# Kernel tuning notes

Hardware: AMD Instinct MI355X
Metric: run time of the kernel (lower is better)

Reference implementation:

```python
import jax, jax.numpy as jnp
import numpy as np

N_HEAD = 16
ROPE_BASE = 10000.0


def setup_inputs() -> dict:
    key = jax.random.key(0)
    k1, k2, k3 = jax.random.split(key, 3)
    B, T, C = 2, 2048, 2048
    x = jax.random.normal(k1, (B, T, C), dtype=jnp.float32)
    # 0.02 init scale keeps attention logits in a sane range
    w_qkv = jax.random.normal(k2, (3 * C, C), dtype=jnp.float32) * 0.02
    w_proj = jax.random.normal(k3, (C, C), dtype=jnp.float32) * 0.02
    return {"x": x, "w_qkv": w_qkv, "w_proj": w_proj}


def _apply_rope(t, cos, sin):
    # t: [B, T, H, hd]; cos/sin: [T, hd//2]
    B, T, H, hd = t.shape
    ts = t.reshape(B, T, H, hd // 2, 2)
    x0, x1 = ts[..., 0], ts[..., 1]
    c = cos[None, :, None, :]
    s = sin[None, :, None, :]
    out = jnp.stack([x0 * c - x1 * s, x1 * c + x0 * s], axis=-1)
    return out.reshape(B, T, H, hd)


def reference(x, w_qkv, w_proj):
    B, T, C = x.shape
    H = N_HEAD
    hd = C // H

    qkv = x @ w_qkv.T                       # [B, T, 3C]
    q, k, v = jnp.split(qkv, 3, axis=2)
    q = q.reshape(B, T, H, hd)
    k = k.reshape(B, T, H, hd)              # present kv: pre-RoPE k, [B,T,H,hd]
    v = v.reshape(B, T, H, hd).transpose(0, 2, 1, 3)  # [B,H,T,hd]

    # RoPE cache (positions = arange(T) since past_key_value is None)
    theta = 1.0 / (ROPE_BASE ** (jnp.arange(0, hd, 2, dtype=jnp.float32) / hd))
    ang = jnp.arange(T, dtype=jnp.float32)[:, None] * theta[None, :]  # [T, hd//2]
    cos, sin = jnp.cos(ang), jnp.sin(ang)

    qr = _apply_rope(q, cos, sin).transpose(0, 2, 1, 3)  # [B,H,T,hd]
    kr = _apply_rope(k, cos, sin).transpose(0, 2, 1, 3)  # [B,H,T,hd]

    scale = 1.0 / jnp.sqrt(jnp.asarray(hd, dtype=qr.dtype))
    scores = jnp.einsum('bhqd,bhkd->bhqk', qr, kr) * scale  # [B,H,T,T]
    attn = jax.nn.softmax(scores, axis=-1)
    o = jnp.einsum('bhqk,bhkd->bhqd', attn, v)              # [B,H,T,hd]
    y = o.transpose(0, 2, 1, 3).reshape(B, T, C) @ w_proj.T
    return (y, k, v)
```

## Files before the change

kernel.cpp:

```cpp
#include <hip/hip_runtime.h>
#include <math.h>


typedef __bf16 bf16_t;
typedef __bf16 bf16x8 __attribute__((ext_vector_type(8)));
typedef __bf16 bf16x4v __attribute__((ext_vector_type(4)));
typedef float  f32x4  __attribute__((ext_vector_type(4)));

#define B_  2
#define T_  2048
#define C_  2048
#define SLICE_ ((size_t)B_ * T_ * C_)

__device__ __forceinline__ void glds16(const void* g, void* l) {
  __builtin_amdgcn_global_load_lds(
      (__attribute__((address_space(1))) void*)(void*)(const_cast<void*>(g)),
      (__attribute__((address_space(3))) void*)(l), 16, 0, 0);
}

__global__ __launch_bounds__(256) void k_cvt(const float4* __restrict__ in,
                                             bf16x4v* __restrict__ out, int n4) {
  int i = blockIdx.x * 256 + threadIdx.x;
  if (i < n4) {
    float4 v = in[i];
    bf16x4v o;
    o[0] = (bf16_t)v.x; o[1] = (bf16_t)v.y; o[2] = (bf16_t)v.z; o[3] = (bf16_t)v.w;
    out[i] = o;
  }
}

__global__ __launch_bounds__(256) void k_tab(float2* __restrict__ tab) {
  int i = blockIdx.x * 256 + threadIdx.x;
  int t = i >> 6, j = i & 63;
  float thf = (float)pow(10000.0, -(double)(2 * j) / 128.0);
  float angf = (float)t * thf;
  double a = (double)angf;
  tab[i] = make_float2((float)cos(a), (float)sin(a));
}

__global__ __launch_bounds__(256, 2) void k_qkv(
    const bf16_t* __restrict__ X, const bf16_t* __restrict__ W,
    const float2* __restrict__ tab,
    bf16_t* __restrict__ qb, bf16_t* __restrict__ kb, bf16_t* __restrict__ vtb,
    float* __restrict__ kout, float* __restrict__ vout) {
  const int K = 2048;
  __shared__ alignas(16) bf16_t smem[17408];
  bf16_t* As = smem;
  bf16_t* Bs = smem + 8192;
  const int tid = threadIdx.x;
  const int lane = tid & 63, wv = tid >> 6;
  const int wm = wv >> 1, wn = wv & 1;
  const int q4 = lane >> 4, l16 = lane & 15;
  const int m0 = blockIdx.x * 128, n0 = blockIdx.y * 128;

  const bf16_t* Ab = X + (size_t)m0 * K;
  const bf16_t* Wb = W + (size_t)n0 * K;

  f32x4 zero4 = {0.f, 0.f, 0.f, 0.f};
  f32x4 acc[4][4];
#pragma unroll
  for (int i = 0; i < 4; ++i)
#pragma unroll
    for (int j = 0; j < 4; ++j) acc[i][j] = zero4;

  for (int k0 = 0; k0 < K; k0 += 64) {
    __syncthreads();
#pragma unroll
    for (int i = 0; i < 4; ++i) {
      int ci = i * 256 + tid;
      glds16(Ab + (size_t)(ci >> 3) * K + k0 + (((ci & 7) ^ ((ci >> 3) & 7)) << 3),
             &As[(i * 256 + wv * 64) * 8]);
    }
#pragma unroll
    for (int i = 0; i < 4; ++i) {
      int ci = i * 256 + tid;
      glds16(Wb + (size_t)(ci >> 3) * K + k0 + (((ci & 7) ^ ((ci >> 3) & 7)) << 3),
             &Bs[(i * 256 + wv * 64) * 8]);
    }
    __syncthreads();
#pragma unroll
    for (int kk = 0; kk < 2; ++kk) {
      bf16x8 afrag[4], bfrag[4];
#pragma unroll
      for (int mf = 0; mf < 4; ++mf)
        afrag[mf] = *(const bf16x8*)&As[(wm * 64 + mf * 16 + l16) * 64 +
                                        ((((kk << 2) | q4) ^ (l16 & 7)) << 3)];
#pragma unroll
      for (int nf = 0; nf < 4; ++nf)
        bfrag[nf] = *(const bf16x8*)&Bs[(wn * 64 + nf * 16 + l16) * 64 +
                                        ((((kk << 2) | q4) ^ (l16 & 7)) << 3)];
#pragma unroll
      for (int mf = 0; mf < 4; ++mf)
#pragma unroll
        for (int nf = 0; nf < 4; ++nf)
          acc[mf][nf] = __builtin_amdgcn_mfma_f32_16x16x32_bf16(
              afrag[mf], bfrag[nf], acc[mf][nf], 0, 0, 0);
    }
  }

  __syncthreads();
  const int sec = n0 >> 11;
  const int t0 = m0 & 2047, bb = m0 >> 11, h = (n0 & 2047) >> 7;

  if (sec < 2) {
#pragma unroll
    for (int mf = 0; mf < 4; ++mf)
#pragma unroll
      for (int nf = 0; nf < 4; ++nf)
#pragma unroll
        for (int r = 0; r < 4; ++r) {
          int ml = wm * 64 + mf * 16 + q4 * 4 + r;
          int d = wn * 64 + nf * 16 + l16;
          float val = acc[mf][nf][r];
          float partner = __shfl_xor(val, 1);
          float2 cs = tab[(t0 + ml) * 64 + (d >> 1)];
          float rv = (d & 1) ? (val * cs.x + partner * cs.y)
                             : (val * cs.x - partner * cs.y);
          if (sec == 0) rv *= 0.08838834764831845f;
          else kout[(size_t)(m0 + ml) * 2048 + h * 128 + d] = val;
          smem[ml * 136 + d] = (bf16_t)rv;
        }
    __syncthreads();
    bf16_t* dst = (sec == 0 ? qb : kb);
    size_t gbase = ((size_t)(bb * 16 + h) * 2048 + t0) * 128;
#pragma unroll
    for (int i = 0; i < 8; ++i) {
      int ci = i * 256 + tid, ml = ci >> 4, cc = (ci & 15) * 8;
      *(bf16x8*)(dst + gbase + (size_t)ml * 128 + cc) =
          *(const bf16x8*)&smem[ml * 136 + cc];
    }
  } else {
#pragma unroll
    for (int mf = 0; mf < 4; ++mf)
#pragma unroll
      for (int nf = 0; nf < 4; ++nf)
#pragma unroll
        for (int r = 0; r < 4; ++r) {
          int ml = wm * 64 + mf * 16 + q4 * 4 + r;
          int d = wn * 64 + nf * 16 + l16;
          float val = acc[mf][nf][r];
          vout[((size_t)(bb * 16 + h) * 2048 + t0 + ml) * 128 + d] = val;
          smem[d * 136 + ml] = (bf16_t)val;
        }
    __syncthreads();
#pragma unroll
    for (int i = 0; i < 8; ++i) {
      int ci = i * 256 + tid, dr = ci >> 4, cc = (ci & 15) * 8;
      *(bf16x8*)(vtb + ((size_t)((bb * 16 + h) * 128 + dr)) * 2048 + t0 + cc) =
          *(const bf16x8*)&smem[dr * 136 + cc];
    }
  }
}

__global__ __launch_bounds__(256, 2) void k_attn(
    const bf16_t* __restrict__ qb, const bf16_t* __restrict__ kb,
    const bf16_t* __restrict__ vtb, bf16_t* __restrict__ ob) {
  __shared__ alignas(16) bf16_t Ps[128 * 80];
  __shared__ alignas(16) bf16_t Ks[64 * 128];
  __shared__ alignas(16) bf16_t Vts[128 * 64];

  const int tid = threadIdx.x;
  const int lane = tid & 63, wv = tid >> 6;
  const int q4 = lane >> 4, l16 = lane & 15;
  const int bh = blockIdx.x >> 4;
  const int q0 = (blockIdx.x & 15) * 128;

  const bf16_t* Qg = qb + (size_t)bh * T_ * 128 + (size_t)q0 * 128;
  const bf16_t* Kg = kb + (size_t)bh * T_ * 128;
  const bf16_t* Vg = vtb + (size_t)bh * 128 * T_;

  bf16x8 qa[2][4];
#pragma unroll
  for (int mf = 0; mf < 2; ++mf)
#pragma unroll
    for (int kf = 0; kf < 4; ++kf)
      qa[mf][kf] = *(const bf16x8*)(Qg + (size_t)(wv * 32 + mf * 16 + l16) * 128 +
                                    kf * 32 + q4 * 8);

  f32x4 zero4 = {0.f, 0.f, 0.f, 0.f};
  float lrow[2][4];
  f32x4 oacc[2][8];
#pragma unroll
  for (int mf = 0; mf < 2; ++mf) {
#pragma unroll
    for (int r = 0; r < 4; ++r) lrow[mf][r] = 0.f;
#pragma unroll
    for (int nf = 0; nf < 8; ++nf) oacc[mf][nf] = zero4;
  }

  for (int key0 = 0; key0 < T_; key0 += 64) {
    __syncthreads();
#pragma unroll
    for (int i = 0; i < 4; ++i) {
      int ci = i * 256 + tid;
      glds16(Kg + (size_t)(key0 + (ci >> 4)) * 128 +
                 (((ci & 15) ^ ((ci >> 4) & 7)) << 3),
             &Ks[(i * 256 + wv * 64) * 8]);
    }
#pragma unroll
    for (int i = 0; i < 4; ++i) {
      int ci = i * 256 + tid;
      glds16(Vg + (size_t)(ci >> 3) * T_ + key0 +
                 (((ci & 7) ^ ((ci >> 3) & 7)) << 3),
             &Vts[(i * 256 + wv * 64) * 8]);
    }
    __syncthreads();

    f32x4 sacc[2][4];
#pragma unroll
    for (int mf = 0; mf < 2; ++mf)
#pragma unroll
      for (int nf = 0; nf < 4; ++nf) sacc[mf][nf] = zero4;
#pragma unroll
    for (int kf = 0; kf < 4; ++kf) {
      bf16x8 bfrag[4];
#pragma unroll
      for (int nf = 0; nf < 4; ++nf)
        bfrag[nf] = *(const bf16x8*)&Ks[(nf * 16 + l16) * 128 +
                                        ((((kf << 2) | q4) ^ (l16 & 7)) << 3)];
#pragma unroll
      for (int mf = 0; mf < 2; ++mf)
#pragma unroll
        for (int nf = 0; nf < 4; ++nf)
          sacc[mf][nf] = __builtin_amdgcn_mfma_f32_16x16x32_bf16(
              qa[mf][kf], bfrag[nf], sacc[mf][nf], 0, 0, 0);
    }

#pragma unroll
    for (int mf = 0; mf < 2; ++mf) {
#pragma unroll
      for (int r = 0; r < 4; ++r) {
        float p0 = __expf(sacc[mf][0][r]);
        float p1 = __expf(sacc[mf][1][r]);
        float p2 = __expf(sacc[mf][2][r]);
        float p3 = __expf(sacc[mf][3][r]);
        int prow = wv * 32 + mf * 16 + q4 * 4 + r;
        Ps[prow * 80 + 0 + l16]  = (bf16_t)p0;
        Ps[prow * 80 + 16 + l16] = (bf16_t)p1;
        Ps[prow * 80 + 32 + l16] = (bf16_t)p2;
        Ps[prow * 80 + 48 + l16] = (bf16_t)p3;
        lrow[mf][r] += (p0 + p1) + (p2 + p3);
      }
    }

#pragma unroll
    for (int kf2 = 0; kf2 < 2; ++kf2) {
      bf16x8 pa[2], vb[8];
#pragma unroll
      for (int mf = 0; mf < 2; ++mf)
        pa[mf] = *(const bf16x8*)&Ps[(wv * 32 + mf * 16 + l16) * 80 +
                                     kf2 * 32 + q4 * 8];
#pragma unroll
      for (int nf = 0; nf < 8; ++nf)
        vb[nf] = *(const bf16x8*)&Vts[(nf * 16 + l16) * 64 +
                                      ((((kf2 << 2) | q4) ^ (l16 & 7)) << 3)];
#pragma unroll
      for (int mf = 0; mf < 2; ++mf)
#pragma unroll
        for (int nf = 0; nf < 8; ++nf)
          oacc[mf][nf] = __builtin_amdgcn_mfma_f32_16x16x32_bf16(
              pa[mf], vb[nf], oacc[mf][nf], 0, 0, 0);
    }
  }

  const int b = bh >> 4, h = bh & 15;
#pragma unroll
  for (int mf = 0; mf < 2; ++mf) {
#pragma unroll
    for (int r = 0; r < 4; ++r) {
      float l = lrow[mf][r];
      l += __shfl_xor(l, 1);
      l += __shfl_xor(l, 2);
      l += __shfl_xor(l, 4);
      l += __shfl_xor(l, 8);
      float inv = 1.f / l;
      int t = q0 + wv * 32 + mf * 16 + q4 * 4 + r;
      size_t base = ((size_t)b * 2048 + t) * 2048 + h * 128;
#pragma unroll
      for (int nf = 0; nf < 8; ++nf)
        ob[base + nf * 16 + l16] = (bf16_t)(oacc[mf][nf][r] * inv);
    }
  }
}

__global__ __launch_bounds__(256, 2) void k_proj(
    const bf16_t* __restrict__ O, const bf16_t* __restrict__ Wp,
    float* __restrict__ Y) {
  const int K = 2048;
  __shared__ alignas(16) bf16_t As[128 * 64];
  __shared__ alignas(16) bf16_t Bs[128 * 64];
  const int tid = threadIdx.x;
  const int lane = tid & 63, wv = tid >> 6;
  const int wm = wv >> 1, wn = wv & 1;
  const int q4 = lane >> 4, l16 = lane & 15;
  const int m0 = blockIdx.x * 128, n0 = blockIdx.y * 128;

  const bf16_t* Ab = O + (size_t)m0 * K;
  const bf16_t* Wb = Wp + (size_t)n0 * K;

  f32x4 zero4 = {0.f, 0.f, 0.f, 0.f};
  f32x4 acc[4][4];
#pragma unroll
  for (int i = 0; i < 4; ++i)
#pragma unroll
    for (int j = 0; j < 4; ++j) acc[i][j] = zero4;

  for (int k0 = 0; k0 < K; k0 += 64) {
    __syncthreads();
#pragma unroll
    for (int i = 0; i < 4; ++i) {
      int ci = i * 256 + tid;
      glds16(Ab + (size_t)(ci >> 3) * K + k0 + (((ci & 7) ^ ((ci >> 3) & 7)) << 3),
             &As[(i * 256 + wv * 64) * 8]);
    }
#pragma unroll
    for (int i = 0; i < 4; ++i) {
      int ci = i * 256 + tid;
      glds16(Wb + (size_t)(ci >> 3) * K + k0 + (((ci & 7) ^ ((ci >> 3) & 7)) << 3),
             &Bs[(i * 256 + wv * 64) * 8]);
    }
    __syncthreads();
#pragma unroll
    for (int kk = 0; kk < 2; ++kk) {
      bf16x8 afrag[4], bfrag[4];
#pragma unroll
      for (int mf = 0; mf < 4; ++mf)
        afrag[mf] = *(const bf16x8*)&As[(wm * 64 + mf * 16 + l16) * 64 +
                                        ((((kk << 2) | q4) ^ (l16 & 7)) << 3)];
#pragma unroll
      for (int nf = 0; nf < 4; ++nf)
        bfrag[nf] = *(const bf16x8*)&Bs[(wn * 64 + nf * 16 + l16) * 64 +
                                        ((((kk << 2) | q4) ^ (l16 & 7)) << 3)];
#pragma unroll
      for (int mf = 0; mf < 4; ++mf)
#pragma unroll
        for (int nf = 0; nf < 4; ++nf)
          acc[mf][nf] = __builtin_amdgcn_mfma_f32_16x16x32_bf16(
              afrag[mf], bfrag[nf], acc[mf][nf], 0, 0, 0);
    }
  }
#pragma unroll
  for (int mf = 0; mf < 4; ++mf)
#pragma unroll
    for (int nf = 0; nf < 4; ++nf)
#pragma unroll
      for (int r = 0; r < 4; ++r) {
        int m = m0 + wm * 64 + mf * 16 + q4 * 4 + r;
        int n = n0 + wn * 64 + nf * 16 + l16;
        Y[(size_t)m * 2048 + n] = acc[mf][nf][r];
      }
}

extern "C" void kernel_launch(void* const* d_in, const int* in_sizes, int n_in,
                              void* d_out, int out_size, void* d_ws, size_t ws_size,
                              hipStream_t stream) {
  const float* x = (const float*)d_in[0];
  const float* wqkv = (const float*)d_in[1];
  const float* wproj = (const float*)d_in[2];

  float* y = (float*)d_out;
  float* kout = y + SLICE_;
  float* vout = y + 2 * SLICE_;

  char* w = (char*)d_ws;
  bf16_t* xb = (bf16_t*)w;      w += SLICE_ * 2;
  bf16_t* wqkvb = (bf16_t*)w;   w += (size_t)12582912 * 2;
  bf16_t* wprojb = (bf16_t*)w;  w += (size_t)4194304 * 2;
  bf16_t* qb = (bf16_t*)w;      w += SLICE_ * 2;
  bf16_t* kb = (bf16_t*)w;      w += SLICE_ * 2;
  bf16_t* vtb = (bf16_t*)w;     w += SLICE_ * 2;
  bf16_t* ob = (bf16_t*)w;      w += SLICE_ * 2;
  float2* tab = (float2*)w;     w += (size_t)131072 * 8;
  (void)ws_size; (void)in_sizes; (void)n_in; (void)out_size;

  k_cvt<<<8192, 256, 0, stream>>>((const float4*)x, (bf16x4v*)xb, 2097152);
  k_cvt<<<12288, 256, 0, stream>>>((const float4*)wqkv, (bf16x4v*)wqkvb, 3145728);
  k_cvt<<<4096, 256, 0, stream>>>((const float4*)wproj, (bf16x4v*)wprojb, 1048576);
  k_tab<<<512, 256, 0, stream>>>(tab);

  dim3 gq(32, 48);
  k_qkv<<<gq, 256, 0, stream>>>(xb, wqkvb, tab, qb, kb, vtb, kout, vout);
  k_attn<<<512, 256, 0, stream>>>(qb, kb, vtb, ob);
  dim3 gp(32, 16);
  k_proj<<<gp, 256, 0, stream>>>(ob, wprojb, y);
}
```

Measured before the change: 395.4 us.

## Rewrite QKV GEMM as 256x256 tile with 8 waves and ping-pong LDS pipeline

Replaces the 128x128, 4-wave QKV GEMM with a 256x256 tile using 512 threads and 128KB of dynamic LDS. Even and odd k-stage buffers are split into halves, and global_load_lds prefetch is interleaved with MFMA phases under raw s_barrier/vmcnt waits and s_setprio. Block IDs are swizzled for L2 locality. This raises operand reuse and hides load latency, at the cost of occupancy (one block per CU with 128KB LDS) and a fragile hand-scheduled barrier sequence. The epilogue is adapted to write two heads per tile.

```diff
diff --git a/kernel.cpp b/kernel.cpp
--- a/kernel.cpp
+++ b/kernel.cpp
@@ -38,116 +38,232 @@
   tab[i] = make_float2((float)cos(a), (float)sin(a));
 }
 
-__global__ __launch_bounds__(256, 2) void k_qkv(
+
+struct FragA { bf16x8 v[4][2]; };
+struct FragB { bf16x8 v[2][2]; };
+
+__device__ __forceinline__ void stage_half(const bf16_t* __restrict__ g, int k0,
+                                           bf16_t* l, int H, int tid) {
+  const int wv = tid >> 6;
+#pragma unroll
+  for (int s = 0; s < 2; ++s) {
+    int ci = s * 512 + tid;
+    int row = ci >> 3;
+    glds16(g + (size_t)(H * 128 + row) * 2048 + k0 + (((ci & 7) ^ (row & 7)) << 3),
+           l + H * 8192 + (size_t)(s * 512 + wv * 64) * 8);
+  }
+}
+
+__device__ __forceinline__ void load_afrags(const bf16_t* buf, int ha, int wm,
+                                            int l16, int q4, FragA& fa) {
+#pragma unroll
+  for (int mf = 0; mf < 4; ++mf) {
+    const bf16_t* rp = buf + (ha * 128 + wm * 64 + mf * 16 + l16) * 64;
+#pragma unroll
+    for (int ks = 0; ks < 2; ++ks)
+      fa.v[mf][ks] = *(const bf16x8*)(rp + ((((ks << 2) | q4) ^ (l16 & 7)) << 3));
+  }
+}
+
+__device__ __forceinline__ void load_bfrags(const bf16_t* buf, int hb, int wn,
+                                            int l16, int q4, FragB& fb) {
+#pragma unroll
+  for (int nf = 0; nf < 2; ++nf) {
+    const bf16_t* rp = buf + (hb * 128 + wn * 32 + nf * 16 + l16) * 64;
+#pragma unroll
+    for (int ks = 0; ks < 2; ++ks)
+      fb.v[nf][ks] = *(const bf16x8*)(rp + ((((ks << 2) | q4) ^ (l16 & 7)) << 3));
+  }
+}
+
+template <int HA, int HB>
+__device__ __forceinline__ void phase_mfma(const FragA& fa, const FragB& fb,
+                                           f32x4 (&acc)[2][4][2][2]) {
+  __builtin_amdgcn_s_setprio(1);
+#pragma unroll
+  for (int ks = 0; ks < 2; ++ks)
+#pragma unroll
+    for (int mf = 0; mf < 4; ++mf)
+#pragma unroll
+      for (int nf = 0; nf < 2; ++nf)
+        acc[HA][mf][HB][nf] = __builtin_amdgcn_mfma_f32_16x16x32_bf16(
+            fa.v[mf][ks], fb.v[nf][ks], acc[HA][mf][HB][nf], 0, 0, 0);
+  __builtin_amdgcn_s_setprio(0);
+}
+
+#define BARRIER() asm volatile("s_barrier" ::: "memory")
+#define VMCNT4()  asm volatile("s_waitcnt vmcnt(4)" ::: "memory")
+
+__global__ __launch_bounds__(512, 2) void k_qkv(
     const bf16_t* __restrict__ X, const bf16_t* __restrict__ W,
     const float2* __restrict__ tab,
     bf16_t* __restrict__ qb, bf16_t* __restrict__ kb, bf16_t* __restrict__ vtb,
     float* __restrict__ kout, float* __restrict__ vout) {
   const int K = 2048;
-  __shared__ alignas(16) bf16_t smem[17408];
-  bf16_t* As = smem;
-  bf16_t* Bs = smem + 8192;
+  extern __shared__ char smem_raw[];
+  bf16_t* sm = (bf16_t*)smem_raw;
+  bf16_t* AE = sm;
+  bf16_t* AO = sm + 16384;
+  bf16_t* BE = sm + 32768;
+  bf16_t* BO = sm + 49152;
+
   const int tid = threadIdx.x;
   const int lane = tid & 63, wv = tid >> 6;
-  const int wm = wv >> 1, wn = wv & 1;
+  const int wm = wv >> 2, wn = wv & 3;
   const int q4 = lane >> 4, l16 = lane & 15;
-  const int m0 = blockIdx.x * 128, n0 = blockIdx.y * 128;
+
+  const int bid = blockIdx.x;
+  const int swz = (bid & 7) * 48 + (bid >> 3);
+  const int m0 = (swz & 15) * 256;
+  const int n0 = (swz >> 4) * 256;
 
   const bf16_t* Ab = X + (size_t)m0 * K;
   const bf16_t* Wb = W + (size_t)n0 * K;
 
-  f32x4 zero4 = {0.f, 0.f, 0.f, 0.f};
-  f32x4 acc[4][4];
-#pragma unroll
-  for (int i = 0; i < 4; ++i)
-#pragma unroll
-    for (int j = 0; j < 4; ++j) acc[i][j] = zero4;
-
-  for (int k0 = 0; k0 < K; k0 += 64) {
-    __syncthreads();
-#pragma unroll
-    for (int i = 0; i < 4; ++i) {
-      int ci = i * 256 + tid;
-      glds16(Ab + (size_t)(ci >> 3) * K + k0 + (((ci & 7) ^ ((ci >> 3) & 7)) << 3),
-             &As[(i * 256 + wv * 64) * 8]);
-    }
-#pragma unroll
-    for (int i = 0; i < 4; ++i) {
-      int ci = i * 256 + tid;
-      glds16(Wb + (size_t)(ci >> 3) * K + k0 + (((ci & 7) ^ ((ci >> 3) & 7)) << 3),
-             &Bs[(i * 256 + wv * 64) * 8]);
-    }
-    __syncthreads();
-#pragma unroll
-    for (int kk = 0; kk < 2; ++kk) {
-      bf16x8 afrag[4], bfrag[4];
+  f32x4 acc[2][4][2][2];
+  {
+    f32x4 zero4 = {0.f, 0.f, 0.f, 0.f};
+#pragma unroll
+    for (int ha = 0; ha < 2; ++ha)
 #pragma unroll
       for (int mf = 0; mf < 4; ++mf)
-        afrag[mf] = *(const bf16x8*)&As[(wm * 64 + mf * 16 + l16) * 64 +
-                                        ((((kk << 2) | q4) ^ (l16 & 7)) << 3)];
-#pragma unroll
-      for (int nf = 0; nf < 4; ++nf)
-        bfrag[nf] = *(const bf16x8*)&Bs[(wn * 64 + nf * 16 + l16) * 64 +
-                                        ((((kk << 2) | q4) ^ (l16 & 7)) << 3)];
+#pragma unroll
+        for (int hb = 0; hb < 2; ++hb)
+#pragma unroll
+          for (int nf = 0; nf < 2; ++nf) acc[ha][mf][hb][nf] = zero4;
+  }
+
+  stage_half(Ab, 0, AE, 0, tid);
+  stage_half(Wb, 0, BE, 0, tid);
+  stage_half(Wb, 0, BE, 1, tid);
+  stage_half(Ab, 0, AE, 1, tid);
+  stage_half(Ab, 64, AO, 0, tid);
+  stage_half(Wb, 64, BO, 1, tid);
+  VMCNT4();
+  BARRIER();
+
+  for (int t = 0; t < 16; ++t) {
+    const int kO  = t * 128 + 64;
+    const int kE2 = (t * 128 + 128) & 2047;
+    const int kO2 = (t * 128 + 192) & 2047;
+
+    FragA fa; FragB fb;
+    load_afrags(AE, 0, wm, l16, q4, fa);
+    load_bfrags(BE, 0, wn, l16, q4, fb);
+    stage_half(Wb, kO, BO, 0, tid);
+    stage_half(Ab, kO, AO, 1, tid);
+    BARRIER();
+    phase_mfma<0, 0>(fa, fb, acc);
+    BARRIER();
+    load_bfrags(BE, 1, wn, l16, q4, fb);
+    BARRIER();
+    phase_mfma<0, 1>(fa, fb, acc);
+    BARRIER();
+    load_afrags(AE, 1, wm, l16, q4, fa);
+    stage_half(Ab, kE2, AE, 0, tid);
+    BARRIER();
+    phase_mfma<1, 1>(fa, fb, acc);
+    BARRIER();
+    load_bfrags(BE, 0, wn, l16, q4, fb);
+    stage_half(Wb, kE2, BE, 1, tid);
+    VMCNT4();
+    BARRIER();
+    phase_mfma<1, 0>(fa, fb, acc);
+    BARRIER();
+    load_afrags(AO, 0, wm, l16, q4, fa);
+    load_bfrags(BO, 0, wn, l16, q4, fb);
+    stage_half(Wb, kE2, BE, 0, tid);
+    stage_half(Ab, kE2, AE, 1, tid);
+    BARRIER();
+    phase_mfma<0, 0>(fa, fb, acc);
+    BARRIER();
+    load_bfrags(BO, 1, wn, l16, q4, fb);
+    BARRIER();
+    phase_mfma<0, 1>(fa, fb, acc);
+    BARRIER();
+    load_afrags(AO, 1, wm, l16, q4, fa);
+    stage_half(Ab, kO2, AO, 0, tid);
+    BARRIER();
+    phase_mfma<1, 1>(fa, fb, acc);
+    BARRIER();
+    load_bfrags(BO, 0, wn, l16, q4, fb);
+    stage_half(Wb, kO2, BO, 1, tid);
+    VMCNT4();
+    BARRIER();
+    phase_mfma<1, 0>(fa, fb, acc);
+    BARRIER();
+  }
+
+  __syncthreads();
+
+  const int sec = n0 >> 11;
+  const int t0 = m0 & 2047, bb = m0 >> 11, h0 = (n0 & 2047) >> 7;
+
+  if (sec < 2) {
+#pragma unroll
+    for (int ha = 0; ha < 2; ++ha) {
+      if (ha) __syncthreads();
 #pragma unroll
       for (int mf = 0; mf < 4; ++mf)
 #pragma unroll
-        for (int nf = 0; nf < 4; ++nf)
-          acc[mf][nf] = __builtin_amdgcn_mfma_f32_16x16x32_bf16(
-              afrag[mf], bfrag[nf], acc[mf][nf], 0, 0, 0);
-    }
-  }
-
-  __syncthreads();
-  const int sec = n0 >> 11;
-  const int t0 = m0 & 2047, bb = m0 >> 11, h = (n0 & 2047) >> 7;
-
-  if (sec < 2) {
-#pragma unroll
-    for (int mf = 0; mf < 4; ++mf)
-#pragma unroll
-      for (int nf = 0; nf < 4; ++nf)
-#pragma unroll
-        for (int r = 0; r < 4; ++r) {
-          int ml = wm * 64 + mf * 16 + q4 * 4 + r;
-          int d = wn * 64 + nf * 16 + l16;
-          float val = acc[mf][nf][r];
-          float partner = __shfl_xor(val, 1);
-          float2 cs = tab[(t0 + ml) * 64 + (d >> 1)];
-          float rv = (d & 1) ? (val * cs.x + partner * cs.y)
-                             : (val * cs.x - partner * cs.y);
-          if (sec == 0) rv *= 0.08838834764831845f;
-          else kout[(size_t)(m0 + ml) * 2048 + h * 128 + d] = val;
-          smem[ml * 136 + d] = (bf16_t)rv;
-        }
-    __syncthreads();
-    bf16_t* dst = (sec == 0 ? qb : kb);
-    size_t gbase = ((size_t)(bb * 16 + h) * 2048 + t0) * 128;
-#pragma unroll
-    for (int i = 0; i < 8; ++i) {
-      int ci = i * 256 + tid, ml = ci >> 4, cc = (ci & 15) * 8;
-      *(bf16x8*)(dst + gbase + (size_t)ml * 128 + cc) =
-          *(const bf16x8*)&smem[ml * 136 + cc];
+        for (int hb = 0; hb < 2; ++hb)
+#pragma unroll
+          for (int nf = 0; nf < 2; ++nf)
+#pragma unroll
+            for (int r = 0; r < 4; ++r) {
+              int mlr = wm * 64 + mf * 16 + q4 * 4 + r;
+              int d2  = hb * 128 + wn * 32 + nf * 16 + l16;
+              int d   = d2 & 127;
+              float val = acc[ha][mf][hb][nf][r];
+              float partner = __shfl_xor(val, 1);
+              float2 cs = tab[(t0 + ha * 128 + mlr) * 64 + (d >> 1)];
+              float rv = (d & 1) ? (val * cs.x + partner * cs.y)
+                                 : (val * cs.x - partner * cs.y);
+              if (sec == 0) rv *= 0.08838834764831845f;
+              else kout[(size_t)(m0 + ha * 128 + mlr) * 2048 +
+                        (h0 + hb) * 128 + d] = val;
+              sm[mlr * 264 + d2] = (bf16_t)rv;
+            }
+      __syncthreads();
+      bf16_t* dst = (sec == 0 ? qb : kb);
+#pragma unroll
+      for (int i = 0; i < 8; ++i) {
+        int ci = i * 512 + tid;
+        int mlr = ci >> 5, cc = (ci & 31) * 8;
+        int hs = cc >> 7, d = cc & 127;
+        *(bf16x8*)(dst +
+                   ((size_t)(bb * 16 + h0 + hs) * 2048 + t0 + ha * 128 + mlr) * 128 +
+                   d) = *(const bf16x8*)&sm[mlr * 264 + cc];
+      }
     }
   } else {
 #pragma unroll
-    for (int mf = 0; mf < 4; ++mf)
-#pragma unroll
-      for (int nf = 0; nf < 4; ++nf)
-#pragma unroll
-        for (int r = 0; r < 4; ++r) {
-          int ml = wm * 64 + mf * 16 + q4 * 4 + r;
-          int d = wn * 64 + nf * 16 + l16;
-          float val = acc[mf][nf][r];
-          vout[((size_t)(bb * 16 + h) * 2048 + t0 + ml) * 128 + d] = val;
-          smem[d * 136 + ml] = (bf16_t)val;
-        }
-    __syncthreads();
-#pragma unroll
-    for (int i = 0; i < 8; ++i) {
-      int ci = i * 256 + tid, dr = ci >> 4, cc = (ci & 15) * 8;
-      *(bf16x8*)(vtb + ((size_t)((bb * 16 + h) * 128 + dr)) * 2048 + t0 + cc) =
-          *(const bf16x8*)&smem[dr * 136 + cc];
+    for (int hb = 0; hb < 2; ++hb) {
+      if (hb) __syncthreads();
+#pragma unroll
+      for (int ha = 0; ha < 2; ++ha)
+#pragma unroll
+        for (int mf = 0; mf < 4; ++mf)
+#pragma unroll
+          for (int nf = 0; nf < 2; ++nf)
+#pragma unroll
+            for (int r = 0; r < 4; ++r) {
+              int ml = ha * 128 + wm * 64 + mf * 16 + q4 * 4 + r;
+              int d2 = hb * 128 + wn * 32 + nf * 16 + l16;
+              int d  = d2 & 127;
+              float val = acc[ha][mf][hb][nf][r];
+              vout[((size_t)(bb * 16 + h0 + hb) * 2048 + t0 + ml) * 128 + d] = val;
+              sm[d * 264 + ml] = (bf16_t)val;
+            }
+      __syncthreads();
+#pragma unroll
+      for (int i = 0; i < 8; ++i) {
+        int ci = i * 512 + tid;
+        int dr = ci >> 5, cc = (ci & 31) * 8;
+        *(bf16x8*)(vtb +
+                   ((size_t)((bb * 16 + h0 + hb) * 128 + dr)) * 2048 + t0 + cc) =
+            *(const bf16x8*)&sm[dr * 264 + cc];
+      }
     }
   }
 }
@@ -373,13 +489,19 @@
   float2* tab = (float2*)w;     w += (size_t)131072 * 8;
   (void)ws_size; (void)in_sizes; (void)n_in; (void)out_size;
 
+  static int smem_set = 0;
+  if (!smem_set) {
+    hipFuncSetAttribute((const void*)k_qkv,
+                        hipFuncAttributeMaxDynamicSharedMemorySize, 131072);
+    smem_set = 1;
+  }
+
   k_cvt<<<8192, 256, 0, stream>>>((const float4*)x, (bf16x4v*)xb, 2097152);
   k_cvt<<<12288, 256, 0, stream>>>((const float4*)wqkv, (bf16x4v*)wqkvb, 3145728);
   k_cvt<<<4096, 256, 0, stream>>>((const float4*)wproj, (bf16x4v*)wprojb, 1048576);
   k_tab<<<512, 256, 0, stream>>>(tab);
 
-  dim3 gq(32, 48);
-  k_qkv<<<gq, 256, 0, stream>>>(xb, wqkvb, tab, qb, kb, vtb, kout, vout);
+  k_qkv<<<384, 512, 131072, stream>>>(xb, wqkvb, tab, qb, kb, vtb, kout, vout);
   k_attn<<<512, 256, 0, stream>>>(qb, kb, vtb, ob);
   dim3 gp(32, 16);
   k_proj<<<gp, 256, 0, stream>>>(ob, wprojb, y);
```

New measurement: 434.9 us. 10.0% more time.

## Fuse prep kernels and register-prefetch next K/V tile in attention

Applied to the files above, without the earlier changes.

Merges the three fp32-to-bf16 conversion launches and the RoPE table launch into one kernel, removing three launches. In the attention kernel, the direct global-to-LDS loads are replaced by loads into registers for the next 64-key tile, issued after the LDS store so they overlap with the current tile's MFMA work. This adds register pressure (eight bf16x8 staging vectors per thread) and changes the LDS write path from async global_load_lds to explicit ds_write.

```diff
diff --git a/kernel.cpp b/kernel.cpp
--- a/kernel.cpp
+++ b/kernel.cpp
@@ -18,24 +18,37 @@
       (__attribute__((address_space(3))) void*)(l), 16, 0, 0);
 }
 
-__global__ __launch_bounds__(256) void k_cvt(const float4* __restrict__ in,
-                                             bf16x4v* __restrict__ out, int n4) {
+__global__ __launch_bounds__(256) void k_prep(
+    const float4* __restrict__ x, const float4* __restrict__ wqkv,
+    const float4* __restrict__ wproj, bf16x4v* __restrict__ xb,
+    bf16x4v* __restrict__ wqkvb, bf16x4v* __restrict__ wprojb,
+    float2* __restrict__ tab) {
   int i = blockIdx.x * 256 + threadIdx.x;
-  if (i < n4) {
-    float4 v = in[i];
+  if (i < 2097152) {
+    float4 v = x[i];
     bf16x4v o;
     o[0] = (bf16_t)v.x; o[1] = (bf16_t)v.y; o[2] = (bf16_t)v.z; o[3] = (bf16_t)v.w;
-    out[i] = o;
-  }
-}
-
-__global__ __launch_bounds__(256) void k_tab(float2* __restrict__ tab) {
-  int i = blockIdx.x * 256 + threadIdx.x;
-  int t = i >> 6, j = i & 63;
-  float thf = (float)pow(10000.0, -(double)(2 * j) / 128.0);
-  float angf = (float)t * thf;
-  double a = (double)angf;
-  tab[i] = make_float2((float)cos(a), (float)sin(a));
+    xb[i] = o;
+  } else if (i < 5242880) {
+    int j = i - 2097152;
+    float4 v = wqkv[j];
+    bf16x4v o;
+    o[0] = (bf16_t)v.x; o[1] = (bf16_t)v.y; o[2] = (bf16_t)v.z; o[3] = (bf16_t)v.w;
+    wqkvb[j] = o;
+  } else if (i < 6291456) {
+    int j = i - 5242880;
+    float4 v = wproj[j];
+    bf16x4v o;
+    o[0] = (bf16_t)v.x; o[1] = (bf16_t)v.y; o[2] = (bf16_t)v.z; o[3] = (bf16_t)v.w;
+    wprojb[j] = o;
+  } else {
+    int j = i - 6291456;
+    int t = j >> 6, jj = j & 63;
+    float thf = (float)pow(10000.0, -(double)(2 * jj) / 128.0);
+    float angf = (float)t * thf;
+    double a = (double)angf;
+    tab[j] = make_float2((float)cos(a), (float)sin(a));
+  }
 }
 
 __global__ __launch_bounds__(256, 2) void k_qkv(
@@ -188,23 +201,38 @@
     for (int nf = 0; nf < 8; ++nf) oacc[mf][nf] = zero4;
   }
 
+  bf16x8 kst[4], vst[4];
+#pragma unroll
+  for (int i = 0; i < 4; ++i) {
+    int ci = i * 256 + tid;
+    kst[i] = *(const bf16x8*)(Kg + (size_t)(ci >> 4) * 128 +
+                              (((ci & 15) ^ ((ci >> 4) & 7)) << 3));
+    vst[i] = *(const bf16x8*)(Vg + (size_t)(ci >> 3) * T_ +
+                              (((ci & 7) ^ ((ci >> 3) & 7)) << 3));
+  }
+
   for (int key0 = 0; key0 < T_; key0 += 64) {
     __syncthreads();
 #pragma unroll
     for (int i = 0; i < 4; ++i) {
       int ci = i * 256 + tid;
-      glds16(Kg + (size_t)(key0 + (ci >> 4)) * 128 +
-                 (((ci & 15) ^ ((ci >> 4) & 7)) << 3),
-             &Ks[(i * 256 + wv * 64) * 8]);
-    }
-#pragma unroll
-    for (int i = 0; i < 4; ++i) {
-      int ci = i * 256 + tid;
-      glds16(Vg + (size_t)(ci >> 3) * T_ + key0 +
-                 (((ci & 7) ^ ((ci >> 3) & 7)) << 3),
-             &Vts[(i * 256 + wv * 64) * 8]);
-    }
-    __syncthreads();
+      *(bf16x8*)&Ks[ci * 8] = kst[i];
+      *(bf16x8*)&Vts[ci * 8] = vst[i];
+    }
+    __syncthreads();
+
+    if (key0 + 64 < T_) {
+      const bf16_t* Kg2 = Kg + (size_t)(key0 + 64) * 128;
+      const bf16_t* Vg2 = Vg + key0 + 64;
+#pragma unroll
+      for (int i = 0; i < 4; ++i) {
+        int ci = i * 256 + tid;
+        kst[i] = *(const bf16x8*)(Kg2 + (size_t)(ci >> 4) * 128 +
+                                  (((ci & 15) ^ ((ci >> 4) & 7)) << 3));
+        vst[i] = *(const bf16x8*)(Vg2 + (size_t)(ci >> 3) * T_ +
+                                  (((ci & 7) ^ ((ci >> 3) & 7)) << 3));
+      }
+    }
 
     f32x4 sacc[2][4];
 #pragma unroll
@@ -373,10 +401,9 @@
   float2* tab = (float2*)w;     w += (size_t)131072 * 8;
   (void)ws_size; (void)in_sizes; (void)n_in; (void)out_size;
 
-  k_cvt<<<8192, 256, 0, stream>>>((const float4*)x, (bf16x4v*)xb, 2097152);
-  k_cvt<<<12288, 256, 0, stream>>>((const float4*)wqkv, (bf16x4v*)wqkvb, 3145728);
-  k_cvt<<<4096, 256, 0, stream>>>((const float4*)wproj, (bf16x4v*)wprojb, 1048576);
-  k_tab<<<512, 256, 0, stream>>>(tab);
+  k_prep<<<25088, 256, 0, stream>>>((const float4*)x, (const float4*)wqkv,
+                                    (const float4*)wproj, (bf16x4v*)xb,
+                                    (bf16x4v*)wqkvb, (bf16x4v*)wprojb, tab);
 
   dim3 gq(32, 48);
   k_qkv<<<gq, 256, 0, stream>>>(xb, wqkvb, tab, qb, kb, vtb, kout, vout);
```

Result: faster. 387.1 us (median of 2 runs) (-2.1%).
